# Optimization experiments

Measured on AMD Instinct MI355X. Metric: run time of the kernel, lower is better.

The kernel has to match this reference:

```python
import jax, jax.numpy as jnp
import numpy as np

N_NODES = 327680      # 8192 graphs * 40 nodes/graph
N_EDGES = 2621440     # avg degree 8
NODES_PER_GRAPH = 40


def _lin(k, fan_in, fan_out):
    s = 1.0 / np.sqrt(fan_in)
    return jax.random.uniform(k, (fan_in, fan_out), jnp.float32, -s, s)


def setup_inputs() -> dict:
    key = jax.random.key(0)
    ks = jax.random.split(key, 12)
    x = jax.random.normal(ks[0], (N_NODES, 58), jnp.float32)
    edge_index = jax.random.randint(ks[1], (2, N_EDGES), 0, N_NODES, dtype=jnp.int32)
    return {
        "x": x,
        "edge_index": edge_index,
        "W1": _lin(ks[2], 58, 96),  "b1": jnp.zeros((96,), jnp.float32),
        "W2": _lin(ks[3], 96, 48),  "b2": jnp.zeros((48,), jnp.float32),
        "l1_w": _lin(ks[4], 40 * 48, 256), "l1_b": jnp.zeros((256,), jnp.float32),
        "l2_w": _lin(ks[5], 256, 64),      "l2_b": jnp.zeros((64,), jnp.float32),
        "l3_w": _lin(ks[6], 64, 1),        "l3_b": jnp.zeros((1,), jnp.float32),
    }


def gcn_conv(x, src, dst, W, b, n):
    # PyG GCNConv: h = X W; out[i] = sum_{(j->i)} d_j^-1/2 d_i^-1/2 h[j] + b
    h = x @ W                                   # [N, out]
    deg = jnp.zeros((n,), h.dtype).at[dst].add(1.0)
    dinv = jnp.where(deg > 0, jax.lax.rsqrt(deg), 0.0)
    norm = dinv[src] * dinv[dst]                # [E]
    out = jax.ops.segment_sum(h[src] * norm[:, None], dst, num_segments=n)
    return out + b


def reference(x, edge_index, W1, b1, W2, b2, l1_w, l1_b, l2_w, l2_b, l3_w, l3_b):
    n = x.shape[0]
    loop = jnp.arange(n, dtype=edge_index.dtype)        # self-loops (PyG default)
    src = jnp.concatenate([edge_index[0], loop])
    dst = jnp.concatenate([edge_index[1], loop])
    h = jax.nn.relu(gcn_conv(x, src, dst, W1, b1, n))   # dropout is identity in eval
    h = jax.nn.relu(gcn_conv(h, src, dst, W2, b2, n))
    g = h.reshape(n // NODES_PER_GRAPH, NODES_PER_GRAPH * 48)
    g = jax.nn.relu(g @ l1_w + l1_b)
    g = jax.nn.relu(g @ l2_w + l2_b)
    return jax.nn.sigmoid(g @ l3_w + l3_b)              # [B, 1]
```

## Files before the change

kernel.cpp:

```cpp
#include <hip/hip_runtime.h>

#define N_NODES 327680
#define N_EDGES 2621440
#define NGRAPH  8192
#define NB      640
#define BCAPE   4608

typedef unsigned int uint;
typedef unsigned short u16;
typedef __attribute__((ext_vector_type(8))) short s16x8;
typedef __attribute__((ext_vector_type(4))) float f32x4;
typedef __attribute__((ext_vector_type(2))) float f32x2;

__device__ __forceinline__ float bl(uint u){ return __uint_as_float(u << 16); }
__device__ __forceinline__ float bh(uint u){ return __uint_as_float(u & 0xffff0000u); }
__device__ __forceinline__ u16 f2b(float f){
    uint u = __float_as_uint(f);
    u += 0x7fffu + ((u>>16)&1u);
    return (u16)(u>>16);
}
__device__ __forceinline__ uint pk(float a, float b){
    return (uint)f2b(a) | ((uint)f2b(b) << 16);
}
__device__ __forceinline__ f32x2 f8lo(uint w){ return __builtin_amdgcn_cvt_pk_f32_fp8((int)w, false); }
__device__ __forceinline__ f32x2 f8hi(uint w){ return __builtin_amdgcn_cvt_pk_f32_fp8((int)w, true); }
__device__ __forceinline__ uint pk4f8(float a, float b, float c, float d){
    int w = __builtin_amdgcn_cvt_pk_fp8_f32(a, b, 0, false);
    w = __builtin_amdgcn_cvt_pk_fp8_f32(c, d, w, true);
    return (uint)w;
}


__device__ void tr_tile(const float* __restrict__ in, u16* __restrict__ out,
                        int K, int N, int Kpad, int kb, int nb){
    __shared__ u16 t[64][72];
    for (int i = threadIdx.x; i < 4096; i += 256){
        int k = i >> 6, n = i & 63;
        int gk = kb + k, gn = nb + n;
        float v = (gk < K && gn < N) ? in[(size_t)gk*N + gn] : 0.f;
        t[n][k] = f2b(v);
    }
    __syncthreads();
    for (int i = threadIdx.x; i < 4096; i += 256){
        int n = i >> 6, k = i & 63;
        int gk = kb + k, gn = nb + n;
        if (gn < N && gk < Kpad) out[(size_t)gn*Kpad + gk] = t[n][k];
    }
}

__global__ __launch_bounds__(256) void k_prep(
    const float* __restrict__ W1, const float* __restrict__ W2,
    const float* __restrict__ l1w, const float* __restrict__ l2w,
    u16* __restrict__ w1t, u16* __restrict__ w2t,
    u16* __restrict__ l1wt, u16* __restrict__ l2wt, int* __restrict__ gcur)
{
    int b = blockIdx.x;
    if (b < 120)      tr_tile(l1w, l1wt, 1920, 256, 1920, (b%30)*64, (b/30)*64);
    else if (b < 124) tr_tile(l2w, l2wt, 256,  64,  256,  (b-120)*64, 0);
    else if (b < 126) tr_tile(W1,  w1t,  58,   96,  64,   0, (b-124)*64);
    else if (b < 128) tr_tile(W2,  w2t,  96,   48,  96,   (b-126)*64, 0);
    else {
        for (int i = threadIdx.x; i < NB; i += 256) gcur[i] = 0;
    }
}


__global__ __launch_bounds__(256) void k_partition(
    const int* __restrict__ src, const int* __restrict__ dst,
    int* __restrict__ gcur, uint* __restrict__ staging)
{
    __shared__ int cnt[NB], base_[NB];
    int tid = threadIdx.x;
    for (int i = tid; i < NB; i += 256) cnt[i] = 0;
    __syncthreads();
    int e0 = blockIdx.x*4096;
    int d[16];
    #pragma unroll
    for (int j = 0; j < 16; ++j){
        d[j] = dst[e0 + j*256 + tid];
        atomicAdd(&cnt[d[j] >> 9], 1);
    }
    __syncthreads();
    for (int i = tid; i < NB; i += 256)
        base_[i] = atomicAdd(&gcur[i], cnt[i]);
    __syncthreads();
    for (int i = tid; i < NB; i += 256) cnt[i] = 0;
    __syncthreads();
    #pragma unroll
    for (int j = 0; j < 16; ++j){
        int e = e0 + j*256 + tid;
        int b = d[j] >> 9;
        int r = atomicAdd(&cnt[b], 1);
        staging[(uint)b*BCAPE + base_[b] + r] = (uint)src[e] | ((uint)(d[j] & 511) << 19);
    }
}


__global__ __launch_bounds__(512) void k_bucket(
    const uint* __restrict__ staging, const int* __restrict__ gcur,
    const float* __restrict__ x,
    int* __restrict__ rowst, int* __restrict__ rendg, float* __restrict__ dinvg,
    int* __restrict__ csr, int* __restrict__ perm, uint* __restrict__ xs32)
{
    __shared__ uint sedge[BCAPE];
    __shared__ int deg[512];
    __shared__ int cur[512];
    __shared__ int wsum[8];
    __shared__ int dh[64], dbase[64];
    __shared__ float sdinv[512];
    const int b = blockIdx.x;
    const int tid = threadIdx.x;
    const int lo = b*BCAPE;
    int cnt = gcur[b];
    if (cnt > BCAPE) cnt = BCAPE;
    deg[tid] = 0;
    if (tid < 64) dh[tid] = 0;
    __syncthreads();
    for (int t = tid; t < cnt; t += 512){
        uint ed = staging[lo + t];
        sedge[t] = ed;
        atomicAdd(&deg[ed >> 19], 1);
    }
    __syncthreads();
    int d = deg[tid];
    int incl = d;
    #pragma unroll
    for (int o = 1; o < 64; o <<= 1){
        int t = __shfl_up(incl, o);
        if ((tid & 63) >= o) incl += t;
    }
    if ((tid & 63) == 63) wsum[tid >> 6] = incl;
    __syncthreads();
    if (tid == 0){
        int a = 0;
        #pragma unroll
        for (int i = 0; i < 8; ++i){ int v = wsum[i]; wsum[i] = a; a += v; }
    }
    __syncthreads();
    incl += wsum[tid >> 6];
    int excl = incl - d;
    int gnode = b*512 + tid;
    float dv = 1.0f / sqrtf((float)(d + 1));
    rowst[gnode] = lo + excl;
    rendg[gnode] = lo + incl;
    dinvg[gnode] = dv;
    sdinv[tid] = dv;
    cur[tid] = lo + excl;
    int bin = min(d, 63);
    atomicAdd(&dh[bin], 1);
    __syncthreads();
    if (tid == 0){
        int a = 0;
        #pragma unroll
        for (int i = 0; i < 64; ++i){ dbase[i] = a; a += dh[i]; dh[i] = 0; }
    }
    __syncthreads();
    int pos = dbase[bin] + atomicAdd(&dh[bin], 1);
    perm[b*512 + pos] = gnode;
    for (int t = tid; t < cnt; t += 512){
        uint ed = sedge[t];
        int p = atomicAdd(&cur[ed >> 19], 1);
        csr[p] = (int)(ed & 0x7FFFFu);
    }
    const size_t n0 = (size_t)b*512;
    for (int i = tid; i < 512*16; i += 512){
        int n = i >> 4, c = i & 15;
        float dvn = sdinv[n];
        float a0 = 0.f, a1 = 0.f, a2 = 0.f, a3 = 0.f;
        int cb = c*4;
        if (cb + 1 < 58){
            float2 v = *(const float2*)&x[(n0 + n)*58 + cb];
            a0 = v.x * dvn; a1 = v.y * dvn;
        }
        if (cb + 3 < 58){
            float2 v = *(const float2*)&x[(n0 + n)*58 + cb + 2];
            a2 = v.x * dvn; a3 = v.y * dvn;
        }
        xs32[(n0 + n)*16 + c] = pk4f8(a0, a1, a2, a3);
    }
}


__global__ __launch_bounds__(256) void k_gather1(
    const int* __restrict__ rs, const int* __restrict__ re,
    const int* __restrict__ csr, const float* __restrict__ dinv,
    const int* __restrict__ perm,
    const uint2* __restrict__ feat2,
    u16* __restrict__ out)
{
    int slot = (blockIdx.x*256 + threadIdx.x) >> 3;
    int c4 = threadIdx.x & 7;
    int node = perm[slot];
    uint2 u = feat2[((uint)node << 3) + c4];
    f32x2 s0 = f8lo(u.x), s1 = f8hi(u.x), s2 = f8lo(u.y), s3 = f8hi(u.y);
    float a0 = s0.x, a1 = s0.y, a2 = s1.x, a3 = s1.y;
    float a4 = s2.x, a5 = s2.y, a6 = s3.x, a7 = s3.y;
    int e = rs[node];
    const int e1 = re[node];
    while (e < e1){
        const int last = e1 - 1;
        int idx[8];
        #pragma unroll
        for (int k = 0; k < 8; ++k) idx[k] = csr[min(e + k, last)];
        uint2 uu[8];
        #pragma unroll
        for (int k = 0; k < 8; ++k) uu[k] = feat2[((uint)idx[k] << 3) + c4];
        #pragma unroll
        for (int k = 0; k < 8; ++k){
            if (e + k < e1){
                f32x2 p0 = f8lo(uu[k].x), p1 = f8hi(uu[k].x);
                f32x2 p2 = f8lo(uu[k].y), p3 = f8hi(uu[k].y);
                a0 += p0.x; a1 += p0.y; a2 += p1.x; a3 += p1.y;
                a4 += p2.x; a5 += p2.y; a6 += p3.x; a7 += p3.y;
            }
        }
        e += 8;
    }
    float di = dinv[node];
    a0 *= di; a1 *= di; a2 *= di; a3 *= di;
    a4 *= di; a5 *= di; a6 *= di; a7 *= di;
    uint4 w;
    w.x = pk(a0,a1); w.y = pk(a2,a3); w.z = pk(a4,a5); w.w = pk(a6,a7);
    *(uint4*)&out[(size_t)node*64 + c4*8] = w;
}


__global__ __launch_bounds__(512) void k_conv_mlp(
    const u16* __restrict__ A,
    const u16* __restrict__ w1t,
    const float* __restrict__ b1,
    const u16* __restrict__ w2t,
    const float* __restrict__ dinv,
    uint* __restrict__ ts32)
{
    __shared__ __align__(16) u16 As[128][72];
    __shared__ __align__(16) u16 Bt1[96][72];
    __shared__ __align__(16) u16 Bt2[48][104];
    __shared__ __align__(16) u16 sh1[128][104];
    __shared__ float sb1[96];
    const int tid = threadIdx.x;
    {
        const u16* Ab = A + (size_t)blockIdx.x*128*64;
        for (int i = tid; i < 1024; i += 512){
            int r = i >> 3, s = i & 7;
            *(uint4*)&As[r][s*8] = *(const uint4*)&Ab[r*64 + s*8];
        }
    }
    for (int i = tid; i < 768; i += 512){
        int n = i >> 3, s = i & 7;
        *(uint4*)&Bt1[n][s*8] = *(const uint4*)&w1t[n*64 + s*8];
    }
    for (int i = tid; i < 576; i += 512){
        int n = i / 12, s = i % 12;
        *(uint4*)&Bt2[n][s*8] = *(const uint4*)&w2t[n*96 + s*8];
    }
    if (tid < 96) sb1[tid] = b1[tid];
    __syncthreads();

    const int wv = tid >> 6, l = tid & 63;
    const int lr = l & 15, lg = l >> 4;
    const int r0 = wv*16;

    f32x4 acc1[6] = {};
    #pragma unroll
    for (int s = 0; s < 2; ++s){
        s16x8 af = *(const s16x8*)&As[r0+lr][s*32 + lg*8];
        #pragma unroll
        for (int t = 0; t < 6; ++t){
            s16x8 bf = *(const s16x8*)&Bt1[t*16+lr][s*32 + lg*8];
            acc1[t] = __builtin_amdgcn_mfma_f32_16x16x32_bf16(af, bf, acc1[t], 0, 0, 0);
        }
    }
    #pragma unroll
    for (int t = 0; t < 6; ++t){
        int col = t*16 + lr;
        float bias = sb1[col];
        #pragma unroll
        for (int r = 0; r < 4; ++r)
            sh1[r0 + lg*4 + r][col] = f2b(fmaxf(acc1[t][r] + bias, 0.f));
    }
    __syncthreads();

    f32x4 acc2[3] = {};
    #pragma unroll
    for (int s = 0; s < 3; ++s){
        s16x8 af = *(const s16x8*)&sh1[r0+lr][s*32 + lg*8];
        #pragma unroll
        for (int t = 0; t < 3; ++t){
            s16x8 bf = *(const s16x8*)&Bt2[t*16+lr][s*32 + lg*8];
            acc2[t] = __builtin_amdgcn_mfma_f32_16x16x32_bf16(af, bf, acc2[t], 0, 0, 0);
        }
    }
    size_t gbase = (size_t)blockIdx.x*128;
    #pragma unroll
    for (int r = 0; r < 4; ++r){
        int row = r0 + lg*4 + r;
        float dv = dinv[gbase + row];
        #pragma unroll
        for (int t = 0; t < 3; ++t)
            sh1[row][t*16 + lr] = f2b(acc2[t][r] * dv);
    }
    __syncthreads();
    #pragma unroll
    for (int it = 0; it < 4; ++it){
        int item = it*64 + l;
        int row = r0 + (item >> 4);
        int c = item & 15;
        uint w = 0;
        if (c < 12){
            float b0 = bl((uint)sh1[row][c*4+0]);
            float b1_ = bl((uint)sh1[row][c*4+1]);
            float b2_ = bl((uint)sh1[row][c*4+2]);
            float b3_ = bl((uint)sh1[row][c*4+3]);
            w = pk4f8(b0, b1_, b2_, b3_);
        }
        ts32[(gbase + row)*16 + c] = w;
    }
}


__global__ __launch_bounds__(256) void k_gather2(
    const int* __restrict__ rs, const int* __restrict__ re,
    const int* __restrict__ csr, const float* __restrict__ dinv,
    const int* __restrict__ perm,
    const uint2* __restrict__ feat2,
    const float* __restrict__ bias,
    u16* __restrict__ out)
{
    int slot = (blockIdx.x*256 + threadIdx.x) >> 3;
    int c4 = threadIdx.x & 7;
    int node = perm[slot];
    uint2 u = feat2[((uint)node << 3) + c4];
    f32x2 s0 = f8lo(u.x), s1 = f8hi(u.x), s2 = f8lo(u.y), s3 = f8hi(u.y);
    float a0 = s0.x, a1 = s0.y, a2 = s1.x, a3 = s1.y;
    float a4 = s2.x, a5 = s2.y, a6 = s3.x, a7 = s3.y;
    int e = rs[node];
    const int e1 = re[node];
    while (e < e1){
        const int last = e1 - 1;
        int idx[8];
        #pragma unroll
        for (int k = 0; k < 8; ++k) idx[k] = csr[min(e + k, last)];
        uint2 uu[8];
        #pragma unroll
        for (int k = 0; k < 8; ++k) uu[k] = feat2[((uint)idx[k] << 3) + c4];
        #pragma unroll
        for (int k = 0; k < 8; ++k){
            if (e + k < e1){
                f32x2 p0 = f8lo(uu[k].x), p1 = f8hi(uu[k].x);
                f32x2 p2 = f8lo(uu[k].y), p3 = f8hi(uu[k].y);
                a0 += p0.x; a1 += p0.y; a2 += p1.x; a3 += p1.y;
                a4 += p2.x; a5 += p2.y; a6 += p3.x; a7 += p3.y;
            }
        }
        e += 8;
    }
    float di = dinv[node];
    if (c4 < 6){
        float4 bz0 = *(const float4*)&bias[8*c4];
        float4 bz1 = *(const float4*)&bias[8*c4 + 4];
        a0 = fmaxf(a0*di + bz0.x, 0.f); a1 = fmaxf(a1*di + bz0.y, 0.f);
        a2 = fmaxf(a2*di + bz0.z, 0.f); a3 = fmaxf(a3*di + bz0.w, 0.f);
        a4 = fmaxf(a4*di + bz1.x, 0.f); a5 = fmaxf(a5*di + bz1.y, 0.f);
        a6 = fmaxf(a6*di + bz1.z, 0.f); a7 = fmaxf(a7*di + bz1.w, 0.f);
        uint4 w;
        w.x = pk(a0,a1); w.y = pk(a2,a3); w.z = pk(a4,a5); w.w = pk(a6,a7);
        *(uint4*)&out[(size_t)node*48 + c4*8] = w;
    }
}


__global__ __launch_bounds__(512) void k_head(
    const u16* __restrict__ A,
    const u16* __restrict__ l1wt,
    const float* __restrict__ l1b,
    const u16* __restrict__ l2wt,
    const float* __restrict__ l2b,
    const float* __restrict__ l3w, const float* __restrict__ l3b,
    float* __restrict__ out)
{
    __shared__ __align__(16) u16 As[32][72];
    __shared__ __align__(16) u16 Bt[256][72];
    __shared__ float part[32][4];
    u16 (*sh1)[264] = (u16(*)[264])&Bt[0][0];
    const int tid = threadIdx.x;
    const int g0 = blockIdx.x*32;
    const int w = tid >> 6, l = tid & 63;
    const int lr = l & 15, lg = l >> 4;
    const int r0 = (w & 1)*16;
    const int c0 = (w >> 1)*64;
    f32x4 acc[4] = {};
    for (int k0 = 0; k0 < 1920; k0 += 64){
        __syncthreads();
        if (tid < 256){
            int r = tid >> 3, s = tid & 7;
            *(uint4*)&As[r][s*8] = *(const uint4*)&A[(size_t)(g0+r)*1920 + k0 + s*8];
        }
        for (int i = tid; i < 2048; i += 512){
            int n = i >> 3, s = i & 7;
            *(uint4*)&Bt[n][s*8] = *(const uint4*)&l1wt[(size_t)n*1920 + k0 + s*8];
        }
        __syncthreads();
        #pragma unroll
        for (int s = 0; s < 2; ++s){
            s16x8 af = *(const s16x8*)&As[r0+lr][s*32 + lg*8];
            #pragma unroll
            for (int t = 0; t < 4; ++t){
                s16x8 bf = *(const s16x8*)&Bt[c0 + t*16 + lr][s*32 + lg*8];
                acc[t] = __builtin_amdgcn_mfma_f32_16x16x32_bf16(af, bf, acc[t], 0, 0, 0);
            }
        }
    }
    __syncthreads();
    #pragma unroll
    for (int t = 0; t < 4; ++t){
        int col = c0 + t*16 + lr;
        float bs = l1b[col];
        #pragma unroll
        for (int r = 0; r < 4; ++r)
            sh1[r0 + lg*4 + r][col] = f2b(fmaxf(acc[t][r] + bs, 0.f));
    }
    __syncthreads();
    f32x4 acc2 = {};
    const int col = (w >> 1)*16 + lr;
    #pragma unroll
    for (int s = 0; s < 8; ++s){
        s16x8 af = *(const s16x8*)&sh1[r0+lr][s*32 + lg*8];
        s16x8 bf = *(const s16x8*)&l2wt[(size_t)col*256 + s*32 + lg*8];
        acc2 = __builtin_amdgcn_mfma_f32_16x16x32_bf16(af, bf, acc2, 0, 0, 0);
    }
    float lb = l2b[col], lw = l3w[col];
    float p[4];
    #pragma unroll
    for (int r = 0; r < 4; ++r)
        p[r] = fmaxf(acc2[r] + lb, 0.f) * lw;
    #pragma unroll
    for (int o = 1; o < 16; o <<= 1){
        #pragma unroll
        for (int r = 0; r < 4; ++r) p[r] += __shfl_xor(p[r], o);
    }
    if (lr == 0){
        #pragma unroll
        for (int r = 0; r < 4; ++r)
            part[r0 + lg*4 + r][w>>1] = p[r];
    }
    __syncthreads();
    if (tid < 32)
        out[g0 + tid] = 1.0f / (1.0f + expf(-(part[tid][0] + part[tid][1]
                                            + part[tid][2] + part[tid][3] + l3b[0])));
}

extern "C" void kernel_launch(void* const* d_in, const int* in_sizes, int n_in,
                              void* d_out, int out_size, void* d_ws, size_t ws_size,
                              hipStream_t stream){
    const float* x   = (const float*)d_in[0];
    const int*   ei  = (const int*)  d_in[1];
    const int*   src = ei;
    const int*   dst = ei + N_EDGES;
    const float* W1  = (const float*)d_in[2];
    const float* b1  = (const float*)d_in[3];
    const float* W2  = (const float*)d_in[4];
    const float* b2  = (const float*)d_in[5];
    const float* l1w = (const float*)d_in[6];
    const float* l1b = (const float*)d_in[7];
    const float* l2w = (const float*)d_in[8];
    const float* l2b = (const float*)d_in[9];
    const float* l3w = (const float*)d_in[10];
    const float* l3b = (const float*)d_in[11];
    float* out = (float*)d_out;

    char* w = (char*)d_ws;
    auto alloc = [&](size_t bytes){ void* p = (void*)w; w += (bytes + 255) & ~(size_t)255; return p; };
    float* dinv    = (float*)alloc((size_t)N_NODES*4);
    int*   rowst   = (int*)  alloc((size_t)N_NODES*4);
    int*   rend    = (int*)  alloc((size_t)N_NODES*4);
    int*   perm    = (int*)  alloc((size_t)N_NODES*4);
    int*   gcur    = (int*)  alloc(NB*4);
    u16*   w1t     = (u16*)  alloc(96*64*2);
    u16*   w2t     = (u16*)  alloc(48*96*2);
    u16*   l1wt    = (u16*)  alloc((size_t)256*1920*2);
    u16*   l2wt    = (u16*)  alloc((size_t)64*256*2);
    int*   csr     = (int*)  alloc((size_t)NB*BCAPE*4);
    uint*  staging = (uint*) alloc((size_t)NB*BCAPE*4);
    char*  BUF_P   = (char*) alloc((size_t)N_NODES*64);
    char*  BUF_Q   = (char*) alloc((size_t)N_NODES*64*2);

    uint* xs32 = (uint*)BUF_P;
    uint* ts32 = (uint*)BUF_P;
    u16*  agg1 = (u16*) BUF_Q;
    u16*  agg2 = (u16*) BUF_Q;

    k_prep     <<<129, 256, 0, stream>>>(W1, W2, l1w, l2w, w1t, w2t, l1wt, l2wt, gcur);

    k_partition<<<640, 256, 0, stream>>>(src, dst, gcur, staging);
    k_bucket   <<<640, 512, 0, stream>>>(staging, gcur, x, rowst, rend, dinv, csr, perm, xs32);

    k_gather1  <<<10240, 256, 0, stream>>>(rowst, rend, csr, dinv, perm,
                                           (const uint2*)xs32, agg1);
    k_conv_mlp <<<2560,  512, 0, stream>>>(agg1, w1t, b1, w2t, dinv, ts32);

    k_gather2  <<<10240, 256, 0, stream>>>(rowst, rend, csr, dinv, perm,
                                           (const uint2*)ts32, b2, agg2);

    k_head     <<<256, 512, 0, stream>>>(agg2, l1wt, l1b, l2wt, l2b, l3w, l3b, out);
}
```

Baseline: 321.0 us.

## Store first-layer aggregate in fp8 and reuse partition atomic ranks

The first gather now packs its normalized aggregates into fp8 instead of bf16, which halves that intermediate buffer's write and read traffic. The conv-MLP kernel unpacks the fp8 values back to bf16 in shared memory. Separately, the partition kernel keeps the rank returned by the first shared-memory atomic, so it drops the counter reset, one barrier and the second atomic pass. The cost is lower precision for the layer-1 activations feeding the matmul.

Measured after the change: 315.8 us. About the same (-1.6%).

```diff
diff --git a/kernel.cpp b/kernel.cpp
--- a/kernel.cpp
+++ b/kernel.cpp
@@ -74,24 +74,21 @@
     for (int i = tid; i < NB; i += 256) cnt[i] = 0;
     __syncthreads();
     int e0 = blockIdx.x*4096;
-    int d[16];
+    int d[16], r[16];
     #pragma unroll
     for (int j = 0; j < 16; ++j){
         d[j] = dst[e0 + j*256 + tid];
-        atomicAdd(&cnt[d[j] >> 9], 1);
+        r[j] = atomicAdd(&cnt[d[j] >> 9], 1);
     }
     __syncthreads();
     for (int i = tid; i < NB; i += 256)
         base_[i] = atomicAdd(&gcur[i], cnt[i]);
-    __syncthreads();
-    for (int i = tid; i < NB; i += 256) cnt[i] = 0;
     __syncthreads();
     #pragma unroll
     for (int j = 0; j < 16; ++j){
         int e = e0 + j*256 + tid;
         int b = d[j] >> 9;
-        int r = atomicAdd(&cnt[b], 1);
-        staging[(uint)b*BCAPE + base_[b] + r] = (uint)src[e] | ((uint)(d[j] & 511) << 19);
+        staging[(uint)b*BCAPE + base_[b] + r[j]] = (uint)src[e] | ((uint)(d[j] & 511) << 19);
     }
 }
 
@@ -186,7 +183,7 @@
     const int* __restrict__ csr, const float* __restrict__ dinv,
     const int* __restrict__ perm,
     const uint2* __restrict__ feat2,
-    u16* __restrict__ out)
+    uint* __restrict__ out)
 {
     int slot = (blockIdx.x*256 + threadIdx.x) >> 3;
     int c4 = threadIdx.x & 7;
@@ -219,14 +216,15 @@
     float di = dinv[node];
     a0 *= di; a1 *= di; a2 *= di; a3 *= di;
     a4 *= di; a5 *= di; a6 *= di; a7 *= di;
-    uint4 w;
-    w.x = pk(a0,a1); w.y = pk(a2,a3); w.z = pk(a4,a5); w.w = pk(a6,a7);
-    *(uint4*)&out[(size_t)node*64 + c4*8] = w;
+    uint2 w;
+    w.x = pk4f8(a0, a1, a2, a3);
+    w.y = pk4f8(a4, a5, a6, a7);
+    *(uint2*)&out[((size_t)node << 4) + c4*2] = w;
 }
 
 
 __global__ __launch_bounds__(512) void k_conv_mlp(
-    const u16* __restrict__ A,
+    const uint* __restrict__ A8,
     const u16* __restrict__ w1t,
     const float* __restrict__ b1,
     const u16* __restrict__ w2t,
@@ -240,10 +238,15 @@
     __shared__ float sb1[96];
     const int tid = threadIdx.x;
     {
-        const u16* Ab = A + (size_t)blockIdx.x*128*64;
-        for (int i = tid; i < 1024; i += 512){
-            int r = i >> 3, s = i & 7;
-            *(uint4*)&As[r][s*8] = *(const uint4*)&Ab[r*64 + s*8];
+        const uint* Ab = A8 + (size_t)blockIdx.x*128*16;
+        for (int i = tid; i < 2048; i += 512){
+            int r = i >> 4, c = i & 15;
+            uint v = Ab[r*16 + c];
+            f32x2 lo = f8lo(v), hi = f8hi(v);
+            uint2 st;
+            st.x = pk(lo.x, lo.y);
+            st.y = pk(hi.x, hi.y);
+            *(uint2*)&As[r][c*4] = st;
         }
     }
     for (int i = tid; i < 768; i += 512){
@@ -487,7 +490,7 @@
 
     uint* xs32 = (uint*)BUF_P;
     uint* ts32 = (uint*)BUF_P;
-    u16*  agg1 = (u16*) BUF_Q;
+    uint* agg1 = (uint*)BUF_Q;
     u16*  agg2 = (u16*) BUF_Q;
 
     k_prep     <<<129, 256, 0, stream>>>(W1, W2, l1w, l2w, w1t, w2t, l1wt, l2wt, gcur);
```
